# Performance work log

Measured on AMD Instinct MI355X. Metric: run time of the kernel, lower is better.

The kernel has to match this reference:

```python
import jax, jax.numpy as jnp
import numpy as np

N = 4096
FEAT = 64


def _pairwise_dist(x):
    # x: [N, F] -> symmetric [N, N] Euclidean distance matrix, zero diagonal
    sq = jnp.sum(x * x, axis=-1)
    d2 = sq[:, None] + sq[None, :] - 2.0 * (x @ x.T)
    d = jnp.sqrt(jnp.maximum(d2, 0.0))
    return d * (1.0 - jnp.eye(x.shape[0], dtype=x.dtype))


def setup_inputs() -> dict:
    key = jax.random.key(0)
    k1, k2 = jax.random.split(key)
    x1 = jax.random.normal(k1, (N, FEAT), dtype=jnp.float32)
    x2 = jax.random.normal(k2, (N, FEAT), dtype=jnp.float32)
    return {"d1": _pairwise_dist(x1), "d2": _pairwise_dist(x2)}


def _mst_edges(d):
    # Prim's algorithm, O(N^2). For a distance matrix with generic (distinct)
    # entries the MST is unique and its N-1 edges are exactly the 0-dim
    # persistence pairs returned by the union-find PersistentHomologyCalculation.
    n = d.shape[0]
    INF = jnp.asarray(jnp.finfo(d.dtype).max, d.dtype)
    in_tree = jnp.zeros((n,), dtype=bool).at[0].set(True)
    min_dist = d[0]                       # best edge weight into the tree per node
    parent = jnp.zeros((n,), dtype=jnp.int32)  # tree endpoint of that best edge

    def step(carry, _):
        in_tree, min_dist, parent = carry
        masked = jnp.where(in_tree, INF, min_dist)
        j = jnp.argmin(masked).astype(jnp.int32)
        edge = jnp.stack([parent[j], j])  # (tree node, new node)
        in_tree = in_tree.at[j].set(True)
        dj = d[j]
        upd = (dj < min_dist) & (~in_tree)
        min_dist = jnp.where(upd, dj, min_dist)
        parent = jnp.where(upd, j, parent)
        return (in_tree, min_dist, parent), edge

    _, edges = jax.lax.scan(step, (in_tree, min_dist, parent), None, length=n - 1)
    return edges  # [N-1, 2] int32; d is symmetric so pair order is irrelevant


def reference(d1, d2):
    # Pairings are computed on detached CPU copies in the original -> no grad
    p1 = _mst_edges(jax.lax.stop_gradient(d1))
    p2 = jax.lax.stop_gradient(_mst_edges(jax.lax.stop_gradient(d2)))
    sig1 = d1[p1[:, 0], p1[:, 1]]
    sig2 = d2[p2[:, 0], p2[:, 1]]
    # match_edges == 'symmetric'
    sig1_2 = d2[p1[:, 0], p1[:, 1]]
    sig2_1 = d1[p2[:, 0], p2[:, 1]]
    return jnp.sum((sig1 - sig1_2) ** 2) + jnp.sum((sig2 - sig2_1) ** 2)
```

## Files before the change

kernel.cpp:

```cpp
#include <hip/hip_runtime.h>
#include <stdint.h>


#define N        4096
#define NROUNDS  12

typedef unsigned long long u64;
typedef uint32_t u32;

#define INFK (~0ull)

struct Ws {
    u64 best[2][N];
    u32 comp[2][N];
    u32 edges[2][N];
    u32 ncomp[2];
    u32 pad[14];
    u64 bm[2][N * 64];
};

__device__ __forceinline__ u64 umin64(u64 a, u64 b) { return a < b ? a : b; }

__device__ __forceinline__ u64 shfl_xor_u64(u64 x, int off) {
    u32 lo = (u32)x, hi = (u32)(x >> 32);
    lo = (u32)__shfl_xor((int)lo, off, 64);
    hi = (u32)__shfl_xor((int)hi, off, 64);
    return ((u64)hi << 32) | lo;
}

__global__ void init_k(Ws* __restrict__ ws) {
    int i = blockIdx.x * blockDim.x + threadIdx.x;
    if (i < N) {
        ws->best[0][i] = INFK; ws->best[1][i] = INFK;
        ws->comp[0][i] = (u32)i; ws->comp[1][i] = (u32)i;
        u32 diag = ((u32)i << 12) | (u32)i;
        ws->edges[0][i] = diag; ws->edges[1][i] = diag;
        if (i < 2) ws->ncomp[i] = (u32)N;
    }
}

__launch_bounds__(256, 4)
__global__ void scanA_k(const float* __restrict__ d1, const float* __restrict__ d2,
                        Ws* __restrict__ ws) {
    const int m = blockIdx.x >> 10;
    const int wave = threadIdx.x >> 6, lane = threadIdx.x & 63;
    const int v = ((blockIdx.x & 1023) << 2) + wave;
    const float4* __restrict__ row4 = (const float4*)((m ? d2 : d1) + (size_t)v * N);
    u64* __restrict__ bmrow = ws->bm[m] + (size_t)v * 64;

    const u32 uv = (u32)v;

    float4 w[16];
    #pragma unroll
    for (int j = 0; j < 16; ++j) w[j] = row4[lane + 64 * j];

    u64 bmin = INFK;
    #pragma unroll
    for (int j = 0; j < 16; ++j) {
        const u32 c0 = (u32)(4 * (lane + 64 * j));
        if (c0 + 0 != uv) bmin = umin64(bmin, (((u64)__float_as_uint(w[j].x)) << 12) | (c0 + 0));
        if (c0 + 1 != uv) bmin = umin64(bmin, (((u64)__float_as_uint(w[j].y)) << 12) | (c0 + 1));
        if (c0 + 2 != uv) bmin = umin64(bmin, (((u64)__float_as_uint(w[j].z)) << 12) | (c0 + 2));
        if (c0 + 3 != uv) bmin = umin64(bmin, (((u64)__float_as_uint(w[j].w)) << 12) | (c0 + 3));
    }

    bmrow[lane] = bmin;

    u64 rowmin = bmin;
    #pragma unroll
    for (int off = 1; off <= 32; off <<= 1)
        rowmin = umin64(rowmin, shfl_xor_u64(rowmin, off));

    if (lane == 0) {
        u32 wb = (u32)(rowmin >> 12);
        u32 u  = (u32)rowmin & 0xFFFu;
        u32 lo = min(uv, u), hi = max(uv, u);
        ws->best[m][v] = ((u64)wb << 24) | ((u64)lo << 12) | (u64)hi;
    }
}

__launch_bounds__(256, 8)
__global__ void scan2_k(const float* __restrict__ d1, const float* __restrict__ d2,
                        Ws* __restrict__ ws) {
    const int m = blockIdx.x >> 10;
    if (ws->ncomp[m] <= 1u) return;
    const int wave = threadIdx.x >> 6, lane = threadIdx.x & 63;
    const int v = ((blockIdx.x & 1023) << 2) + wave;

    const float* __restrict__ dm = m ? d2 : d1;
    const u32*   __restrict__ cm = ws->comp[m];
    u64* __restrict__ bmrow = ws->bm[m] + (size_t)v * 64;

    const u32 cv = cm[v];
    u64 key = bmrow[lane];
    bool cross = false;
    if (key != INFK) cross = (cm[(u32)key & 0xFFFu] != cv);

    u64 kb = cross ? key : INFK;
    #pragma unroll
    for (int off = 1; off <= 32; off <<= 1)
        kb = umin64(kb, shfl_xor_u64(kb, off));

    const bool need = (!cross) && (key < kb);
    u64 nm = INFK;
    if (need) {
        const float4* __restrict__ row4 = (const float4*)(dm + (size_t)v * N);
        const uint4*  __restrict__ c4   = (const uint4*)cm;
        #pragma unroll
        for (int j = 0; j < 16; ++j) {
            const int c = lane + 64 * j;
            float4 w = row4[c];
            uint4 cu = c4[c];
            u32 c0 = (u32)(4 * c);
            if (cu.x != cv) nm = umin64(nm, (((u64)__float_as_uint(w.x)) << 12) | (c0 + 0));
            if (cu.y != cv) nm = umin64(nm, (((u64)__float_as_uint(w.y)) << 12) | (c0 + 1));
            if (cu.z != cv) nm = umin64(nm, (((u64)__float_as_uint(w.z)) << 12) | (c0 + 2));
            if (cu.w != cv) nm = umin64(nm, (((u64)__float_as_uint(w.w)) << 12) | (c0 + 3));
        }
        bmrow[lane] = nm;
    }
    u64 kb2 = need ? nm : INFK;
    #pragma unroll
    for (int off = 1; off <= 32; off <<= 1)
        kb2 = umin64(kb2, shfl_xor_u64(kb2, off));

    u64 fin = umin64(kb, kb2);
    if (lane == 0 && fin != INFK) {
        u32 wb = (u32)(fin >> 12);
        u32 u  = (u32)fin & 0xFFFu;
        u32 lo = min((u32)v, u), hi = max((u32)v, u);
        u64 g  = ((u64)wb << 24) | ((u64)lo << 12) | (u64)hi;
        if (g < ws->best[m][cv])
            atomicMin(&ws->best[m][cv], g);
    }
}

__launch_bounds__(256, 8)
__global__ void scanF_k(const float* __restrict__ d1, const float* __restrict__ d2,
                        Ws* __restrict__ ws, int first) {
    const int m = blockIdx.x >> 10;
    if (ws->ncomp[m] <= 1u) return;
    const int wave = threadIdx.x >> 6, lane = threadIdx.x & 63;
    const int v = ((blockIdx.x & 1023) << 2) + wave;
    const float* __restrict__ dm = m ? d2 : d1;
    const u32*   __restrict__ cm = ws->comp[m];
    const float4* __restrict__ row4 = (const float4*)(dm + (size_t)v * N);
    const uint4*  __restrict__ c4   = (const uint4*)cm;
    const u32 cv = first ? (u32)v : cm[v];
    u64 kmin = INFK;
    #pragma unroll
    for (int j = 0; j < 16; ++j) {
        const int c = lane + 64 * j;
        float4 w = row4[c];
        uint4 cu;
        if (!first) cu = c4[c];
        const u32 c0 = (u32)(4 * c);
        bool x0, x1, x2, x3;
        if (first) {
            const u32 uvv = (u32)v;
            x0 = (c0+0 != uvv); x1 = (c0+1 != uvv); x2 = (c0+2 != uvv); x3 = (c0+3 != uvv);
        } else {
            x0 = (cu.x != cv); x1 = (cu.y != cv); x2 = (cu.z != cv); x3 = (cu.w != cv);
        }
        if (x0) kmin = umin64(kmin, (((u64)__float_as_uint(w.x)) << 12) | (c0 + 0));
        if (x1) kmin = umin64(kmin, (((u64)__float_as_uint(w.y)) << 12) | (c0 + 1));
        if (x2) kmin = umin64(kmin, (((u64)__float_as_uint(w.z)) << 12) | (c0 + 2));
        if (x3) kmin = umin64(kmin, (((u64)__float_as_uint(w.w)) << 12) | (c0 + 3));
    }
    #pragma unroll
    for (int off = 1; off <= 32; off <<= 1)
        kmin = umin64(kmin, shfl_xor_u64(kmin, off));
    if (lane == 0 && kmin != INFK) {
        u32 wb = (u32)(kmin >> 12);
        u32 u  = (u32)kmin & 0xFFFu;
        u32 lo = min((u32)v, u), hi = max((u32)v, u);
        u64 g  = ((u64)wb << 24) | ((u64)lo << 12) | (u64)hi;
        if (first) ws->best[m][v] = g;
        else if (g < ws->best[m][cv]) atomicMin(&ws->best[m][cv], g);
    }
}

__launch_bounds__(1024, 1)
__global__ void hook_k(Ws* __restrict__ ws) {
    const int m = blockIdx.x;
    const int tid = threadIdx.x;
    if (ws->ncomp[m] <= 1u) return;

    u32* __restrict__ gcomp = ws->comp[m];
    u64* __restrict__ best  = ws->best[m];

    __shared__ u32 compL[N];
    __shared__ u32 nxtA[N];
    __shared__ u32 nxtB[N];
    __shared__ u32 red[16];

    {
        uint4* dst = (uint4*)compL;
        const uint4* src = (const uint4*)gcomp;
        if (tid < N / 4) dst[tid] = src[tid];
    }
    __syncthreads();

    bool isroot[4];
    u64  bkey[4];

    #pragma unroll
    for (int k = 0; k < 4; ++k) {
        int i = tid + k * 1024;
        u32 x = (u32)i;
        bool r = (compL[i] == (u32)i);
        isroot[k] = r;
        u64 g = 0;
        if (r) {
            g = best[i];
            u32 lo = (u32)(g >> 12) & 0xFFFu;
            u32 hi = (u32)g & 0xFFFu;
            u32 cl = compL[lo], ch = compL[hi];
            x = (cl == (u32)i) ? ch : cl;
        }
        bkey[k] = g;
        nxtA[i] = x;
    }
    __syncthreads();

    #pragma unroll
    for (int k = 0; k < 4; ++k) {
        int i = tid + k * 1024;
        u32 nn = (u32)i;
        if (isroot[k]) {
            u32 o = nxtA[i];
            bool mutual = (nxtA[o] == (u32)i);
            nn = (mutual && ((u32)i < o)) ? (u32)i : o;
            if (nn != (u32)i)
                ws->edges[m][i] = (u32)(bkey[k] & 0xFFFFFFu);
        }
        nxtB[i] = nn;
    }
    __syncthreads();

    for (int s = 0; s < 12; ++s) {
        #pragma unroll
        for (int k = 0; k < 4; ++k) {
            int i = tid + k * 1024;
            nxtB[i] = nxtB[nxtB[i]];
        }
        __syncthreads();
    }

    u32 cnt = 0;
    #pragma unroll
    for (int k = 0; k < 4; ++k) {
        int i = tid + k * 1024;
        if (isroot[k] && nxtB[i] == (u32)i) cnt++;
    }
    #pragma unroll
    for (int off = 32; off >= 1; off >>= 1) cnt += (u32)__shfl_down((int)cnt, off, 64);
    const int lane = tid & 63, wave = tid >> 6;
    if (lane == 0) red[wave] = cnt;
    __syncthreads();

    #pragma unroll
    for (int k = 0; k < 4; ++k) {
        int i = tid + k * 1024;
        gcomp[i] = nxtB[compL[i]];
        if (isroot[k]) best[i] = INFK;
    }
    if (tid == 0) {
        u32 t = 0;
        #pragma unroll
        for (int w = 0; w < 16; ++w) t += red[w];
        ws->ncomp[m] = t;
    }
}

__launch_bounds__(256, 1)
__global__ void epi_k(const float* __restrict__ d1, const float* __restrict__ d2,
                      Ws* __restrict__ ws, float* __restrict__ out) {
    const int m = blockIdx.x, tid = threadIdx.x;
    float acc = 0.f;
    for (int i = tid; i < N; i += 256) {
        u32 pk = ws->edges[m][i];
        u32 lo = (pk >> 12) & 0xFFFu, hi = pk & 0xFFFu;
        size_t off = (size_t)lo * N + hi;
        float df = d1[off] - d2[off];
        acc += df * df;
    }
    #pragma unroll
    for (int off = 32; off >= 1; off >>= 1) acc += __shfl_down(acc, off, 64);
    __shared__ float part[4];
    const int lane = tid & 63, wave = tid >> 6;
    if (lane == 0) part[wave] = acc;
    __syncthreads();
    if (tid == 0) atomicAdd(out, part[0] + part[1] + part[2] + part[3]);
}

extern "C" void kernel_launch(void* const* d_in, const int* in_sizes, int n_in,
                              void* d_out, int out_size, void* d_ws, size_t ws_size,
                              hipStream_t stream) {
    (void)in_sizes; (void)n_in; (void)out_size;
    const float* d1 = (const float*)d_in[0];
    const float* d2 = (const float*)d_in[1];
    float* out = (float*)d_out;
    Ws* ws = (Ws*)d_ws;
    const bool big = (ws_size >= sizeof(Ws));

    hipMemsetAsync(d_out, 0, sizeof(float), stream);
    init_k<<<dim3(16), dim3(256), 0, stream>>>(ws);
    for (int r = 0; r < NROUNDS; ++r) {
        if (big) {
            if (r == 0) scanA_k<<<dim3(2048), dim3(256), 0, stream>>>(d1, d2, ws);
            else        scan2_k<<<dim3(2048), dim3(256), 0, stream>>>(d1, d2, ws);
        } else {
            scanF_k<<<dim3(2048), dim3(256), 0, stream>>>(d1, d2, ws, r == 0 ? 1 : 0);
        }
        hook_k<<<dim3(2), dim3(1024), 0, stream>>>(ws);
    }
    epi_k<<<dim3(2), dim3(256), 0, stream>>>(d1, d2, ws, out);
}
```

Measured before the change: 282.4 us.

## Fold init into first scan, epilogue into last hook, early-exit pointer jumping

```diff
diff --git a/kernel.cpp b/kernel.cpp
--- a/kernel.cpp
+++ b/kernel.cpp
@@ -28,43 +28,27 @@
     return ((u64)hi << 32) | lo;
 }
 
-__global__ void init_k(Ws* __restrict__ ws) {
-    int i = blockIdx.x * blockDim.x + threadIdx.x;
-    if (i < N) {
-        ws->best[0][i] = INFK; ws->best[1][i] = INFK;
-        ws->comp[0][i] = (u32)i; ws->comp[1][i] = (u32)i;
-        u32 diag = ((u32)i << 12) | (u32)i;
-        ws->edges[0][i] = diag; ws->edges[1][i] = diag;
-        if (i < 2) ws->ncomp[i] = (u32)N;
-    }
-}
-
-__launch_bounds__(256, 4)
+__launch_bounds__(256, 8)
 __global__ void scanA_k(const float* __restrict__ d1, const float* __restrict__ d2,
                         Ws* __restrict__ ws) {
     const int m = blockIdx.x >> 10;
     const int wave = threadIdx.x >> 6, lane = threadIdx.x & 63;
     const int v = ((blockIdx.x & 1023) << 2) + wave;
     const float4* __restrict__ row4 = (const float4*)((m ? d2 : d1) + (size_t)v * N);
-    u64* __restrict__ bmrow = ws->bm[m] + (size_t)v * 64;
 
     const u32 uv = (u32)v;
-
-    float4 w[16];
-    #pragma unroll
-    for (int j = 0; j < 16; ++j) w[j] = row4[lane + 64 * j];
-
     u64 bmin = INFK;
     #pragma unroll
     for (int j = 0; j < 16; ++j) {
-        const u32 c0 = (u32)(4 * (lane + 64 * j));
-        if (c0 + 0 != uv) bmin = umin64(bmin, (((u64)__float_as_uint(w[j].x)) << 12) | (c0 + 0));
-        if (c0 + 1 != uv) bmin = umin64(bmin, (((u64)__float_as_uint(w[j].y)) << 12) | (c0 + 1));
-        if (c0 + 2 != uv) bmin = umin64(bmin, (((u64)__float_as_uint(w[j].z)) << 12) | (c0 + 2));
-        if (c0 + 3 != uv) bmin = umin64(bmin, (((u64)__float_as_uint(w[j].w)) << 12) | (c0 + 3));
-    }
-
-    bmrow[lane] = bmin;
+        const int c = lane + 64 * j;
+        float4 w = row4[c];
+        const u32 c0 = (u32)(4 * c);
+        if (c0 + 0 != uv) bmin = umin64(bmin, (((u64)__float_as_uint(w.x)) << 12) | (c0 + 0));
+        if (c0 + 1 != uv) bmin = umin64(bmin, (((u64)__float_as_uint(w.y)) << 12) | (c0 + 1));
+        if (c0 + 2 != uv) bmin = umin64(bmin, (((u64)__float_as_uint(w.z)) << 12) | (c0 + 2));
+        if (c0 + 3 != uv) bmin = umin64(bmin, (((u64)__float_as_uint(w.w)) << 12) | (c0 + 3));
+    }
+    ws->bm[m][(size_t)v * 64 + lane] = bmin;
 
     u64 rowmin = bmin;
     #pragma unroll
@@ -72,11 +56,15 @@
         rowmin = umin64(rowmin, shfl_xor_u64(rowmin, off));
 
     if (lane == 0) {
-        u32 wb = (u32)(rowmin >> 12);
         u32 u  = (u32)rowmin & 0xFFFu;
+        u64 wb = rowmin >> 12;
         u32 lo = min(uv, u), hi = max(uv, u);
-        ws->best[m][v] = ((u64)wb << 24) | ((u64)lo << 12) | (u64)hi;
-    }
+        ws->best[m][v]  = (wb << 24) | ((u64)lo << 12) | (u64)hi;
+        ws->comp[m][v]  = uv;
+        ws->edges[m][v] = (uv << 12) | uv;
+    }
+    if (threadIdx.x == 0 && (blockIdx.x & 1023) == 0)
+        ws->ncomp[m] = (u32)N;
 }
 
 __launch_bounds__(256, 8)
@@ -126,10 +114,10 @@
 
     u64 fin = umin64(kb, kb2);
     if (lane == 0 && fin != INFK) {
-        u32 wb = (u32)(fin >> 12);
         u32 u  = (u32)fin & 0xFFFu;
+        u64 wb = fin >> 12;
         u32 lo = min((u32)v, u), hi = max((u32)v, u);
-        u64 g  = ((u64)wb << 24) | ((u64)lo << 12) | (u64)hi;
+        u64 g  = (wb << 24) | ((u64)lo << 12) | (u64)hi;
         if (g < ws->best[m][cv])
             atomicMin(&ws->best[m][cv], g);
     }
@@ -139,7 +127,7 @@
 __global__ void scanF_k(const float* __restrict__ d1, const float* __restrict__ d2,
                         Ws* __restrict__ ws, int first) {
     const int m = blockIdx.x >> 10;
-    if (ws->ncomp[m] <= 1u) return;
+    if (!first && ws->ncomp[m] <= 1u) return;
     const int wave = threadIdx.x >> 6, lane = threadIdx.x & 63;
     const int v = ((blockIdx.x & 1023) << 2) + wave;
     const float* __restrict__ dm = m ? d2 : d1;
@@ -157,8 +145,7 @@
         const u32 c0 = (u32)(4 * c);
         bool x0, x1, x2, x3;
         if (first) {
-            const u32 uvv = (u32)v;
-            x0 = (c0+0 != uvv); x1 = (c0+1 != uvv); x2 = (c0+2 != uvv); x3 = (c0+3 != uvv);
+            x0 = (c0+0 != cv); x1 = (c0+1 != cv); x2 = (c0+2 != cv); x3 = (c0+3 != cv);
         } else {
             x0 = (cu.x != cv); x1 = (cu.y != cv); x2 = (cu.z != cv); x3 = (cu.w != cv);
         }
@@ -171,127 +158,144 @@
     for (int off = 1; off <= 32; off <<= 1)
         kmin = umin64(kmin, shfl_xor_u64(kmin, off));
     if (lane == 0 && kmin != INFK) {
-        u32 wb = (u32)(kmin >> 12);
         u32 u  = (u32)kmin & 0xFFFu;
+        u64 wb = kmin >> 12;
         u32 lo = min((u32)v, u), hi = max((u32)v, u);
-        u64 g  = ((u64)wb << 24) | ((u64)lo << 12) | (u64)hi;
-        if (first) ws->best[m][v] = g;
-        else if (g < ws->best[m][cv]) atomicMin(&ws->best[m][cv], g);
-    }
+        u64 g  = (wb << 24) | ((u64)lo << 12) | (u64)hi;
+        if (first) {
+            ws->best[m][v]  = g;
+            ws->comp[m][v]  = (u32)v;
+            ws->edges[m][v] = ((u32)v << 12) | (u32)v;
+        } else if (g < ws->best[m][cv]) {
+            atomicMin(&ws->best[m][cv], g);
+        }
+    }
+    if (first && threadIdx.x == 0 && (blockIdx.x & 1023) == 0)
+        ws->ncomp[m] = (u32)N;
 }
 
 __launch_bounds__(1024, 1)
-__global__ void hook_k(Ws* __restrict__ ws) {
+__global__ void hook_k(const float* __restrict__ d1, const float* __restrict__ d2,
+                       Ws* __restrict__ ws, float* __restrict__ out, int fin) {
     const int m = blockIdx.x;
     const int tid = threadIdx.x;
-    if (ws->ncomp[m] <= 1u) return;
-
-    u32* __restrict__ gcomp = ws->comp[m];
-    u64* __restrict__ best  = ws->best[m];
+    const int lane = tid & 63, wave = tid >> 6;
 
     __shared__ u32 compL[N];
     __shared__ u32 nxtA[N];
     __shared__ u32 nxtB[N];
     __shared__ u32 red[16];
-
-    {
-        uint4* dst = (uint4*)compL;
-        const uint4* src = (const uint4*)gcomp;
-        if (tid < N / 4) dst[tid] = src[tid];
-    }
-    __syncthreads();
-
-    bool isroot[4];
-    u64  bkey[4];
-
-    #pragma unroll
-    for (int k = 0; k < 4; ++k) {
-        int i = tid + k * 1024;
-        u32 x = (u32)i;
-        bool r = (compL[i] == (u32)i);
-        isroot[k] = r;
-        u64 g = 0;
-        if (r) {
-            g = best[i];
-            u32 lo = (u32)(g >> 12) & 0xFFFu;
-            u32 hi = (u32)g & 0xFFFu;
-            u32 cl = compL[lo], ch = compL[hi];
-            x = (cl == (u32)i) ? ch : cl;
-        }
-        bkey[k] = g;
-        nxtA[i] = x;
-    }
-    __syncthreads();
-
-    #pragma unroll
-    for (int k = 0; k < 4; ++k) {
-        int i = tid + k * 1024;
-        u32 nn = (u32)i;
-        if (isroot[k]) {
-            u32 o = nxtA[i];
-            bool mutual = (nxtA[o] == (u32)i);
-            nn = (mutual && ((u32)i < o)) ? (u32)i : o;
-            if (nn != (u32)i)
-                ws->edges[m][i] = (u32)(bkey[k] & 0xFFFFFFu);
-        }
-        nxtB[i] = nn;
-    }
-    __syncthreads();
-
-    for (int s = 0; s < 12; ++s) {
-        #pragma unroll
-        for (int k = 0; k < 4; ++k) {
-            int i = tid + k * 1024;
-            nxtB[i] = nxtB[nxtB[i]];
-        }
-        __syncthreads();
-    }
-
-    u32 cnt = 0;
-    #pragma unroll
-    for (int k = 0; k < 4; ++k) {
-        int i = tid + k * 1024;
-        if (isroot[k] && nxtB[i] == (u32)i) cnt++;
-    }
-    #pragma unroll
-    for (int off = 32; off >= 1; off >>= 1) cnt += (u32)__shfl_down((int)cnt, off, 64);
-    const int lane = tid & 63, wave = tid >> 6;
-    if (lane == 0) red[wave] = cnt;
-    __syncthreads();
-
-    #pragma unroll
-    for (int k = 0; k < 4; ++k) {
-        int i = tid + k * 1024;
-        gcomp[i] = nxtB[compL[i]];
-        if (isroot[k]) best[i] = INFK;
-    }
-    if (tid == 0) {
-        u32 t = 0;
-        #pragma unroll
-        for (int w = 0; w < 16; ++w) t += red[w];
-        ws->ncomp[m] = t;
-    }
-}
-
-__launch_bounds__(256, 1)
-__global__ void epi_k(const float* __restrict__ d1, const float* __restrict__ d2,
-                      Ws* __restrict__ ws, float* __restrict__ out) {
-    const int m = blockIdx.x, tid = threadIdx.x;
-    float acc = 0.f;
-    for (int i = tid; i < N; i += 256) {
-        u32 pk = ws->edges[m][i];
-        u32 lo = (pk >> 12) & 0xFFFu, hi = pk & 0xFFFu;
-        size_t off = (size_t)lo * N + hi;
-        float df = d1[off] - d2[off];
-        acc += df * df;
-    }
-    #pragma unroll
-    for (int off = 32; off >= 1; off >>= 1) acc += __shfl_down(acc, off, 64);
-    __shared__ float part[4];
-    const int lane = tid & 63, wave = tid >> 6;
-    if (lane == 0) part[wave] = acc;
-    __syncthreads();
-    if (tid == 0) atomicAdd(out, part[0] + part[1] + part[2] + part[3]);
+    __shared__ float fpart[16];
+
+    if (ws->ncomp[m] > 1u) {
+        u32* __restrict__ gcomp = ws->comp[m];
+        u64* __restrict__ best  = ws->best[m];
+
+        {
+            uint4* dst = (uint4*)compL;
+            const uint4* src = (const uint4*)gcomp;
+            if (tid < N / 4) dst[tid] = src[tid];
+        }
+        __syncthreads();
+
+        bool isroot[4];
+        u64  bkey[4];
+
+        #pragma unroll
+        for (int k = 0; k < 4; ++k) {
+            int i = tid + k * 1024;
+            u32 x = (u32)i;
+            bool r = (compL[i] == (u32)i);
+            isroot[k] = r;
+            u64 g = 0;
+            if (r) {
+                g = best[i];
+                u32 lo = (u32)(g >> 12) & 0xFFFu;
+                u32 hi = (u32)g & 0xFFFu;
+                u32 cl = compL[lo], ch = compL[hi];
+                x = (cl == (u32)i) ? ch : cl;
+            }
+            bkey[k] = g;
+            nxtA[i] = x;
+        }
+        __syncthreads();
+
+        #pragma unroll
+        for (int k = 0; k < 4; ++k) {
+            int i = tid + k * 1024;
+            u32 nn = (u32)i;
+            if (isroot[k]) {
+                u32 o = nxtA[i];
+                bool mutual = (nxtA[o] == (u32)i);
+                nn = (mutual && ((u32)i < o)) ? (u32)i : o;
+                if (nn != (u32)i)
+                    ws->edges[m][i] = (u32)(bkey[k] & 0xFFFFFFu);
+            }
+            nxtB[i] = nn;
+        }
+        __syncthreads();
+
+        for (int s = 0; s < 12; ++s) {
+            u32 changed = 0;
+            #pragma unroll
+            for (int k = 0; k < 4; ++k) {
+                int i = tid + k * 1024;
+                u32 a = nxtB[i];
+                u32 t = nxtB[a];
+                if (t != a) changed = 1u;
+                nxtB[i] = t;
+            }
+            if (!__syncthreads_or((int)changed)) break;
+        }
+
+        u32 cnt = 0;
+        #pragma unroll
+        for (int k = 0; k < 4; ++k) {
+            int i = tid + k * 1024;
+            if (isroot[k] && nxtB[i] == (u32)i) cnt++;
+        }
+        #pragma unroll
+        for (int off = 32; off >= 1; off >>= 1) cnt += (u32)__shfl_down((int)cnt, off, 64);
+        if (lane == 0) red[wave] = cnt;
+        __syncthreads();
+
+        #pragma unroll
+        for (int k = 0; k < 4; ++k) {
+            int i = tid + k * 1024;
+            gcomp[i] = nxtB[compL[i]];
+            if (isroot[k]) best[i] = INFK;
+        }
+        if (tid == 0) {
+            u32 t = 0;
+            #pragma unroll
+            for (int w = 0; w < 16; ++w) t += red[w];
+            ws->ncomp[m] = t;
+        }
+    }
+
+    if (fin) {
+        __syncthreads();
+        float acc = 0.f;
+        #pragma unroll
+        for (int k = 0; k < 4; ++k) {
+            int i = tid + k * 1024;
+            u32 pk = ws->edges[m][i];
+            u32 lo = (pk >> 12) & 0xFFFu, hi = pk & 0xFFFu;
+            size_t off = (size_t)lo * N + hi;
+            float df = d1[off] - d2[off];
+            acc += df * df;
+        }
+        #pragma unroll
+        for (int off = 32; off >= 1; off >>= 1) acc += __shfl_down(acc, off, 64);
+        if (lane == 0) fpart[wave] = acc;
+        __syncthreads();
+        if (tid == 0) {
+            float t = 0.f;
+            #pragma unroll
+            for (int w = 0; w < 16; ++w) t += fpart[w];
+            atomicAdd(out, t);
+        }
+    }
 }
 
 extern "C" void kernel_launch(void* const* d_in, const int* in_sizes, int n_in,
@@ -305,7 +309,6 @@
     const bool big = (ws_size >= sizeof(Ws));
 
     hipMemsetAsync(d_out, 0, sizeof(float), stream);
-    init_k<<<dim3(16), dim3(256), 0, stream>>>(ws);
     for (int r = 0; r < NROUNDS; ++r) {
         if (big) {
             if (r == 0) scanA_k<<<dim3(2048), dim3(256), 0, stream>>>(d1, d2, ws);
@@ -313,7 +316,6 @@
         } else {
             scanF_k<<<dim3(2048), dim3(256), 0, stream>>>(d1, d2, ws, r == 0 ? 1 : 0);
         }
-        hook_k<<<dim3(2), dim3(1024), 0, stream>>>(ws);
-    }
-    epi_k<<<dim3(2), dim3(256), 0, stream>>>(d1, d2, ws, out);
-}
+        hook_k<<<dim3(2), dim3(1024), 0, stream>>>(d1, d2, ws, out, r == NROUNDS - 1 ? 1 : 0);
+    }
+}
```

Measured after the change: 262.7 us. -7.0%, faster.
